# Performance work log

Hardware: AMD Instinct MI355X
Metric: run time of the kernel (lower is better)

The kernel has to match this reference:

```python
import jax, jax.numpy as jnp
import numpy as np

N_NODES = 100_000
N_EDGES = 1_600_000
D_IN, D_HID, N_CLASSES = 128, 128, 40


def setup_inputs() -> dict:
    key = jax.random.key(0)
    ks = jax.random.split(key, 8)
    x = jax.random.normal(ks[0], (N_NODES, D_IN), dtype=jnp.float32)
    edge_index = jax.random.randint(ks[1], (2, N_EDGES), 0, N_NODES, dtype=jnp.int64)
    dims = [(D_IN, D_HID), (D_HID, D_HID), (D_HID, N_CLASSES)]
    inp = {"x": x, "edge_index": edge_index}
    for i, (di, do) in enumerate(dims):
        s = 1.0 / np.sqrt(di)
        inp[f"W_l{i}"] = jax.random.normal(ks[2 + 2 * i], (di, do), dtype=jnp.float32) * s
        inp[f"W_r{i}"] = jax.random.normal(ks[3 + 2 * i], (di, do), dtype=jnp.float32) * s
        inp[f"b{i}"] = jnp.zeros((do,), dtype=jnp.float32)
    return inp


def _sage_conv(x, src, dst, deg_inv, W_l, W_r, b):
    # gather messages from source nodes, mean-aggregate at target nodes
    msg = x[src]                                        # [E, d_in]
    aggr = jax.ops.segment_sum(msg, dst, num_segments=N_NODES) * deg_inv  # [N, d_in]
    return aggr @ W_l + b + x @ W_r                     # [N, d_out]


def reference(x, edge_index, W_l0, W_r0, b0, W_l1, W_r1, b1, W_l2, W_r2, b2):
    src, dst = edge_index[0], edge_index[1]
    deg = jax.ops.segment_sum(jnp.ones((N_EDGES,), x.dtype), dst, num_segments=N_NODES)
    deg_inv = (1.0 / jnp.maximum(deg, 1.0))[:, None]    # [N, 1]

    h = _sage_conv(x, src, dst, deg_inv, W_l0, W_r0, b0)
    h = jax.nn.relu(h)  # dropout p=0.3 is identity in eval mode
    h = _sage_conv(h, src, dst, deg_inv, W_l1, W_r1, b1)
    h = jax.nn.relu(h)
    h = _sage_conv(h, src, dst, deg_inv, W_l2, W_r2, b2)
    return jax.nn.log_softmax(h, axis=1)
```

## Files before the change

### kernel.cpp

```cpp
#include <hip/hip_runtime.h>
#include <math.h>

#define THREADS 256
#define BSHIFT 8
#define BSIZE 256
#define NEB 512

typedef short short8 __attribute__((ext_vector_type(8)));
typedef float f32x4 __attribute__((ext_vector_type(4)));

__device__ __forceinline__ unsigned short f2bf(float f) {
  unsigned u = __builtin_bit_cast(unsigned, f);
  return (unsigned short)((u + 0x7FFFu + ((u >> 16) & 1u)) >> 16);
}
__device__ __forceinline__ float bflo(unsigned u) {
  return __builtin_bit_cast(float, u << 16);
}
__device__ __forceinline__ float bfhi(unsigned u) {
  return __builtin_bit_cast(float, u & 0xFFFF0000u);
}
__device__ __forceinline__ unsigned pack2(float x, float y) {
  return (unsigned)f2bf(x) | ((unsigned)f2bf(y) << 16);
}

__device__ __forceinline__ void acc8(float* a, uint4 u) {
  a[0] += bflo(u.x); a[1] += bfhi(u.x);
  a[2] += bflo(u.y); a[3] += bfhi(u.y);
  a[4] += bflo(u.z); a[5] += bfhi(u.z);
  a[6] += bflo(u.w); a[7] += bfhi(u.w);
}


__global__ __launch_bounds__(256) void k_ehist(const int* __restrict__ dst,
                                               int* __restrict__ cnt_bm,
                                               int E, int chunk, int nbk) {
  __shared__ int h[1024];
  int blk = blockIdx.x, t = threadIdx.x;
  for (int i = t; i < nbk; i += 256) h[i] = 0;
  __syncthreads();
  int e0 = blk * chunk, e1 = min(e0 + chunk, E);
  for (int e = e0 + t; e < e1; e += 256) atomicAdd(&h[dst[e] >> BSHIFT], 1);
  __syncthreads();
  for (int i = t; i < nbk; i += 256) cnt_bm[(size_t)blk * nbk + i] = h[i];
}

__global__ __launch_bounds__(256) void k_bktscan(const int* __restrict__ cnt_bm,
                                                 int* __restrict__ locoff_tm,
                                                 int* __restrict__ bktot, int nbk) {
  int g = blockIdx.x, t = threadIdx.x;
  int c0 = cnt_bm[(size_t)(2 * t) * nbk + g];
  int c1 = cnt_bm[(size_t)(2 * t + 1) * nbk + g];
  __shared__ int sh[256];
  int s = c0 + c1;
  sh[t] = s;
  __syncthreads();
  for (int off = 1; off < 256; off <<= 1) {
    int v = (t >= off) ? sh[t - off] : 0;
    __syncthreads();
    if (t >= off) sh[t] += v;
    __syncthreads();
  }
  int excl = sh[t] - s;
  ((int2*)(locoff_tm + (size_t)g * NEB))[t] = make_int2(excl, excl + c0);
  if (t == 255) bktot[g] = sh[255];
}

__global__ __launch_bounds__(256) void k_topscan(const int* __restrict__ bktot,
                                                 int* __restrict__ bucket_base,
                                                 int nbk, int E,
                                                 int* __restrict__ row_ptr, int N) {
  __shared__ int sums[256];
  int t = threadIdx.x;
  int vals[4];
  int s = 0;
#pragma unroll
  for (int j = 0; j < 4; ++j) {
    int idx = t * 4 + j;
    vals[j] = (idx < nbk) ? bktot[idx] : 0;
    s += vals[j];
  }
  sums[t] = s;
  __syncthreads();
  for (int off = 1; off < 256; off <<= 1) {
    int v = (t >= off) ? sums[t - off] : 0;
    __syncthreads();
    if (t >= off) sums[t] += v;
    __syncthreads();
  }
  int run = sums[t] - s;
#pragma unroll
  for (int j = 0; j < 4; ++j) {
    int idx = t * 4 + j;
    if (idx < nbk) bucket_base[idx] = run;
    run += vals[j];
  }
  if (t == 0) { bucket_base[nbk] = E; row_ptr[N] = E; }
}

__global__ __launch_bounds__(256) void k_eplace(const int* __restrict__ src,
                                                const int* __restrict__ dst,
                                                const int* __restrict__ bucket_base,
                                                const int* __restrict__ locoff_tm,
                                                int* __restrict__ bedge,
                                                int E, int chunk, int nbk) {
  __shared__ int lptr[1024];
  int blk = blockIdx.x, t = threadIdx.x;
  for (int i = t; i < nbk; i += 256)
    lptr[i] = bucket_base[i] + locoff_tm[(size_t)i * NEB + blk];
  __syncthreads();
  int e0 = blk * chunk, e1 = min(e0 + chunk, E);
  for (int e = e0 + t; e < e1; e += 256) {
    int d = dst[e];
    int b = d >> BSHIFT;
    int p = atomicAdd(&lptr[b], 1);
    bedge[p] = (src[e] << 8) | (d & (BSIZE - 1));
  }
}

__global__ __launch_bounds__(256) void k_bcsr2(const int* __restrict__ bedge,
                                               const int* __restrict__ bucket_base,
                                               int* __restrict__ row_ptr,
                                               int* __restrict__ col, int N) {
  int g = blockIdx.x, t = threadIdx.x;
  int beg = bucket_base[g], end = bucket_base[g + 1];
  __shared__ int deg[BSIZE];
  __shared__ int sh[BSIZE];
  __shared__ int cur[BSIZE];
  deg[t] = 0;
  __syncthreads();
  for (int i = beg + t; i < end; i += 256)
    atomicAdd(&deg[bedge[i] & (BSIZE - 1)], 1);
  __syncthreads();
  int s = deg[t];
  sh[t] = s;
  __syncthreads();
  for (int off = 1; off < 256; off <<= 1) {
    int v = (t >= off) ? sh[t - off] : 0;
    __syncthreads();
    if (t >= off) sh[t] += v;
    __syncthreads();
  }
  int ex = beg + sh[t] - s;
  int node = g * BSIZE + t;
  if (node < N) row_ptr[node] = ex;
  cur[t] = ex;
  __syncthreads();
  for (int i = beg + t; i < end; i += 256) {
    int ed = bedge[i];
    int p = atomicAdd(&cur[ed & (BSIZE - 1)], 1);
    col[p] = ed >> 8;
  }
}

__global__ __launch_bounds__(256) void k_wswz_all(
    const float* __restrict__ Wl0, const float* __restrict__ Wr0,
    const float* __restrict__ Wl1, const float* __restrict__ Wr1,
    const float* __restrict__ Wl2, const float* __restrict__ Wr2,
    unsigned short* __restrict__ out0, unsigned short* __restrict__ out1,
    unsigned short* __restrict__ out2) {
  int b = blockIdx.x, t = threadIdx.x;
  if (b < 256) {
    const float* Wl = (b < 128) ? Wl0 : Wl1;
    const float* Wr = (b < 128) ? Wr0 : Wr1;
    unsigned short* out = (b < 128) ? out0 : out1;
    int idx = (b & 127) * 256 + t;
    int j = idx & 7, lane = (idx >> 3) & 63, ct = (idx >> 9) & 15, ks = idx >> 13;
    int k = ks * 32 + (lane >> 4) * 8 + j;
    int c = ct * 16 + (lane & 15);
    float v = (c < 128) ? Wl[k * 128 + c] : Wr[k * 128 + (c - 128)];
    out[idx] = f2bf(v);
  } else {
    int idx = (b - 256) * 256 + t;
    int j = idx & 7, lane = (idx >> 3) & 63;
    int tile = idx >> 9;
    int ct = tile % 5, ks = tile / 5;
    int k = ks * 32 + (lane >> 4) * 8 + j;
    int c = ct * 16 + (lane & 15);
    float v = (c < 40) ? Wl2[k * 40 + c] : ((c < 80) ? Wr2[k * 40 + (c - 40)] : 0.f);
    out2[idx] = f2bf(v);
  }
}

__device__ __forceinline__ void gemm128_body(
    const short8 xf[4], const short8 xg[4],
    const unsigned short* __restrict__ Wswz, const float* __restrict__ bias,
    unsigned short* __restrict__ outL, unsigned short* __restrict__ outR,
    int M, int wave, int lane,
    unsigned short (*lt)[16][136], int rb0) {
  int quad = lane >> 4, n16 = lane & 15;
#pragma unroll
  for (int ct = 0; ct < 8; ++ct) {
    f32x4 accA = {0.f, 0.f, 0.f, 0.f};
    f32x4 accB = {0.f, 0.f, 0.f, 0.f};
    const unsigned short* wp = Wswz + (size_t)(ct * 64 + lane) * 8;
#pragma unroll
    for (int ks = 0; ks < 4; ++ks) {
      short8 wf = *(const short8*)(wp + ks * 8192);
      accA = __builtin_amdgcn_mfma_f32_16x16x32_bf16(wf, xf[ks], accA, 0, 0, 0);
      accB = __builtin_amdgcn_mfma_f32_16x16x32_bf16(wf, xg[ks], accB, 0, 0, 0);
    }
    int ch = ct * 16 + quad * 4;
    ushort4 oA, oB;
    oA.x = f2bf(accA[0]); oA.y = f2bf(accA[1]); oA.z = f2bf(accA[2]); oA.w = f2bf(accA[3]);
    oB.x = f2bf(accB[0]); oB.y = f2bf(accB[1]); oB.z = f2bf(accB[2]); oB.w = f2bf(accB[3]);
    *(ushort4*)&lt[0][n16][ch] = oA;
    *(ushort4*)&lt[1][n16][ch] = oB;
  }
#pragma unroll
  for (int r = 0; r < 4; ++r) {
    int nd = r * 4 + (lane >> 4);
    int ic = (lane & 15) * 8;
    uint4 vA = *(const uint4*)&lt[0][nd][ic];
    uint4 vB = *(const uint4*)&lt[1][nd][ic];
    if (rb0 + nd < M)      *(uint4*)(outL + ((size_t)(rb0 + nd)) * 128 + ic) = vA;
    if (rb0 + 64 + nd < M) *(uint4*)(outL + ((size_t)(rb0 + 64 + nd)) * 128 + ic) = vB;
  }
#pragma unroll
  for (int ct = 8; ct < 16; ++ct) {
    f32x4 accA = {0.f, 0.f, 0.f, 0.f};
    f32x4 accB = {0.f, 0.f, 0.f, 0.f};
    const unsigned short* wp = Wswz + (size_t)(ct * 64 + lane) * 8;
#pragma unroll
    for (int ks = 0; ks < 4; ++ks) {
      short8 wf = *(const short8*)(wp + ks * 8192);
      accA = __builtin_amdgcn_mfma_f32_16x16x32_bf16(wf, xf[ks], accA, 0, 0, 0);
      accB = __builtin_amdgcn_mfma_f32_16x16x32_bf16(wf, xg[ks], accB, 0, 0, 0);
    }
    int ch = (ct - 8) * 16 + quad * 4;
    float4 bv = *(const float4*)(bias + ch);
    ushort4 oA, oB;
    oA.x = f2bf(accA[0] + bv.x); oA.y = f2bf(accA[1] + bv.y);
    oA.z = f2bf(accA[2] + bv.z); oA.w = f2bf(accA[3] + bv.w);
    oB.x = f2bf(accB[0] + bv.x); oB.y = f2bf(accB[1] + bv.y);
    oB.z = f2bf(accB[2] + bv.z); oB.w = f2bf(accB[3] + bv.w);
    *(ushort4*)&lt[0][n16][ch] = oA;
    *(ushort4*)&lt[1][n16][ch] = oB;
  }
#pragma unroll
  for (int r = 0; r < 4; ++r) {
    int nd = r * 4 + (lane >> 4);
    int ic = (lane & 15) * 8;
    uint4 vA = *(const uint4*)&lt[0][nd][ic];
    uint4 vB = *(const uint4*)&lt[1][nd][ic];
    if (rb0 + nd < M)      *(uint4*)(outR + ((size_t)(rb0 + nd)) * 128 + ic) = vA;
    if (rb0 + 64 + nd < M) *(uint4*)(outR + ((size_t)(rb0 + 64 + nd)) * 128 + ic) = vB;
  }
}

__global__ __launch_bounds__(256) void gemm128_mfma_x32(
    const float* __restrict__ X, const unsigned short* __restrict__ Wswz,
    const float* __restrict__ bias,
    unsigned short* __restrict__ outL, unsigned short* __restrict__ outR, int M) {
  __shared__ __align__(16) unsigned short lt[4][2][16][136];
  int wave = threadIdx.x >> 6, lane = threadIdx.x & 63;
  int quad = lane >> 4, n16 = lane & 15;
  int rowA = blockIdx.x * 128 + wave * 16 + n16;
  int rA = min(rowA, M - 1), rB = min(rowA + 64, M - 1);

  short8 xf[4], xg[4];
  const float* xpA = X + (size_t)rA * 128 + quad * 8;
  const float* xpB = X + (size_t)rB * 128 + quad * 8;
#pragma unroll
  for (int ks = 0; ks < 4; ++ks) {
    float4 a0 = *(const float4*)(xpA + ks * 32);
    float4 a1 = *(const float4*)(xpA + ks * 32 + 4);
    float4 b0 = *(const float4*)(xpB + ks * 32);
    float4 b1 = *(const float4*)(xpB + ks * 32 + 4);
    short8 f, g;
    f[0] = (short)f2bf(a0.x); f[1] = (short)f2bf(a0.y);
    f[2] = (short)f2bf(a0.z); f[3] = (short)f2bf(a0.w);
    f[4] = (short)f2bf(a1.x); f[5] = (short)f2bf(a1.y);
    f[6] = (short)f2bf(a1.z); f[7] = (short)f2bf(a1.w);
    g[0] = (short)f2bf(b0.x); g[1] = (short)f2bf(b0.y);
    g[2] = (short)f2bf(b0.z); g[3] = (short)f2bf(b0.w);
    g[4] = (short)f2bf(b1.x); g[5] = (short)f2bf(b1.y);
    g[6] = (short)f2bf(b1.z); g[7] = (short)f2bf(b1.w);
    xf[ks] = f;
    xg[ks] = g;
  }
  gemm128_body(xf, xg, Wswz, bias, outL, outR, M, wave, lane,
               lt[wave], blockIdx.x * 128 + wave * 16);
}

__global__ __launch_bounds__(256) void gemm128_mfma(
    const unsigned short* __restrict__ Xb, const unsigned short* __restrict__ Wswz,
    const float* __restrict__ bias,
    unsigned short* __restrict__ outL, unsigned short* __restrict__ outR, int M) {
  __shared__ __align__(16) unsigned short lt[4][2][16][136];
  int wave = threadIdx.x >> 6, lane = threadIdx.x & 63;
  int quad = lane >> 4, n16 = lane & 15;
  int rowA = blockIdx.x * 128 + wave * 16 + n16;
  int rA = min(rowA, M - 1), rB = min(rowA + 64, M - 1);

  short8 xf[4], xg[4];
  const unsigned short* xpA = Xb + (size_t)rA * 128 + quad * 8;
  const unsigned short* xpB = Xb + (size_t)rB * 128 + quad * 8;
#pragma unroll
  for (int ks = 0; ks < 4; ++ks) {
    xf[ks] = *(const short8*)(xpA + ks * 32);
    xg[ks] = *(const short8*)(xpB + ks * 32);
  }
  gemm128_body(xf, xg, Wswz, bias, outL, outR, M, wave, lane,
               lt[wave], blockIdx.x * 128 + wave * 16);
}

__global__ __launch_bounds__(256) void gemm40_mfma(
    const unsigned short* __restrict__ Xb, const unsigned short* __restrict__ Wswz,
    const float* __restrict__ bias,
    unsigned short* __restrict__ tlb, float* __restrict__ tr, int M) {
  int wave = threadIdx.x >> 6, lane = threadIdx.x & 63;
  int quad = lane >> 4, n16 = lane & 15;
  int row = blockIdx.x * 64 + wave * 16 + n16;
  int row_ld = min(row, M - 1);
  bool ok = row < M;

  short8 xf[4];
  const unsigned short* xp = Xb + (size_t)row_ld * 128 + quad * 8;
#pragma unroll
  for (int ks = 0; ks < 4; ++ks) xf[ks] = *(const short8*)(xp + ks * 32);

#pragma unroll
  for (int ct = 0; ct < 5; ++ct) {
    f32x4 acc = {0.f, 0.f, 0.f, 0.f};
    const unsigned short* wp = Wswz + (size_t)(ct * 64 + lane) * 8;
#pragma unroll
    for (int ks = 0; ks < 4; ++ks) {
      short8 wf = *(const short8*)(wp + (size_t)ks * 5 * 64 * 8);
      acc = __builtin_amdgcn_mfma_f32_16x16x32_bf16(wf, xf[ks], acc, 0, 0, 0);
    }
    int cglob = ct * 16 + quad * 4;
    if (!ok) continue;
    if (cglob < 40) {
      ushort4 o;
      o.x = f2bf(acc[0]); o.y = f2bf(acc[1]); o.z = f2bf(acc[2]); o.w = f2bf(acc[3]);
      *(ushort4*)(tlb + (size_t)row * 64 + cglob) = o;
    } else {
      int c = cglob - 40;
      float4 bv = *(const float4*)(bias + c);
      float4 o;
      o.x = acc[0] + bv.x; o.y = acc[1] + bv.y;
      o.z = acc[2] + bv.z; o.w = acc[3] + bv.w;
      *(float4*)(tr + (size_t)row * 40 + c) = o;
    }
  }
}

__global__ __launch_bounds__(256) void agg128b(
    const unsigned short* __restrict__ xl, const unsigned short* __restrict__ xr,
    const int* __restrict__ row_ptr, const int* __restrict__ col,
    unsigned short* __restrict__ h, int Nn) {
  int wave = threadIdx.x >> 6;
  int lane = threadIdx.x & 63;
  int pair = lane >> 5;
  int l32 = lane & 31;
  int n = blockIdx.x * 4 + wave;
  if (n >= Nn) return;
  int beg = row_ptr[n], end = row_ptr[n + 1];
  int deg = end - beg;
  const uint2* xlq = (const uint2*)xl;
  float a0x = 0.f, a0y = 0.f, a0z = 0.f, a0w = 0.f;
  float a1x = 0.f, a1y = 0.f, a1z = 0.f, a1w = 0.f;
  float a2x = 0.f, a2y = 0.f, a2z = 0.f, a2w = 0.f;
  float a3x = 0.f, a3y = 0.f, a3z = 0.f, a3w = 0.f;
  int e = beg + pair;
  for (int it = deg >> 3; it > 0; --it, e += 8) {
    uint2 u0 = xlq[(size_t)col[e]     * 32 + l32];
    uint2 u1 = xlq[(size_t)col[e + 2] * 32 + l32];
    uint2 u2 = xlq[(size_t)col[e + 4] * 32 + l32];
    uint2 u3 = xlq[(size_t)col[e + 6] * 32 + l32];
    a0x += bflo(u0.x); a0y += bfhi(u0.x); a0z += bflo(u0.y); a0w += bfhi(u0.y);
    a1x += bflo(u1.x); a1y += bfhi(u1.x); a1z += bflo(u1.y); a1w += bfhi(u1.y);
    a2x += bflo(u2.x); a2y += bfhi(u2.x); a2z += bflo(u2.y); a2w += bfhi(u2.y);
    a3x += bflo(u3.x); a3y += bfhi(u3.x); a3z += bflo(u3.y); a3w += bfhi(u3.y);
  }
  for (; e < end; e += 2) {
    uint2 u = xlq[(size_t)col[e] * 32 + l32];
    a0x += bflo(u.x); a0y += bfhi(u.x); a0z += bflo(u.y); a0w += bfhi(u.y);
  }
  float ax = (a0x + a1x) + (a2x + a3x);
  float ay = (a0y + a1y) + (a2y + a3y);
  float az = (a0z + a1z) + (a2z + a3z);
  float aw = (a0w + a1w) + (a2w + a3w);
  ax += __shfl_xor(ax, 32);
  ay += __shfl_xor(ay, 32);
  az += __shfl_xor(az, 32);
  aw += __shfl_xor(aw, 32);
  if (pair == 0) {
    float di = 1.0f / (float)max(deg, 1);
    uint2 r = ((const uint2*)xr)[(size_t)n * 32 + l32];
    float ox = fmaxf(fmaf(ax, di, bflo(r.x)), 0.f);
    float oy = fmaxf(fmaf(ay, di, bfhi(r.x)), 0.f);
    float oz = fmaxf(fmaf(az, di, bflo(r.y)), 0.f);
    float ow = fmaxf(fmaf(aw, di, bfhi(r.y)), 0.f);
    uint2 o;
    o.x = pack2(ox, oy);
    o.y = pack2(oz, ow);
    ((uint2*)h)[(size_t)n * 32 + l32] = o;
  }
}

__global__ __launch_bounds__(256) void agg40_lsm(
    const unsigned short* __restrict__ tlb, const float* __restrict__ tr,
    const int* __restrict__ row_ptr, const int* __restrict__ col,
    float* __restrict__ out, int Nn) {
  int wave = threadIdx.x >> 6;
  int lane = threadIdx.x & 63;
  int ew = lane >> 3;
  int l8 = lane & 7;
  int n = blockIdx.x * 4 + wave;
  if (n >= Nn) return;
  int beg = row_ptr[n], end = row_ptr[n + 1];
  int deg = end - beg;
  const uint4* tlq = (const uint4*)tlb;
  float a0[8], a1[8];
#pragma unroll
  for (int j = 0; j < 8; ++j) { a0[j] = 0.f; a1[j] = 0.f; }
  int rounds = (deg + 15) >> 4;
  if (rounds > 0) {
    int end1 = end - 1;
    int e = beg + ew;
    int c0 = col[min(e, end1)];
    int c1 = col[min(e + 8, end1)];
    for (int it = rounds - 1; it > 0; --it) {
      uint4 u0 = tlq[(size_t)c0 * 8 + l8];
      uint4 u1 = tlq[(size_t)c1 * 8 + l8];
      int en = e + 16;
      int cn0 = col[min(en, end1)];
      int cn1 = col[min(en + 8, end1)];
      acc8(a0, u0); acc8(a1, u1);
      c0 = cn0; c1 = cn1; e = en;
    }
    uint4 u0 = tlq[(size_t)c0 * 8 + l8];
    uint4 u1 = tlq[(size_t)c1 * 8 + l8];
    uint4 z = make_uint4(0u, 0u, 0u, 0u);
    if (e >= end) u0 = z;
    if (e + 8 >= end) u1 = z;
    acc8(a0, u0); acc8(a1, u1);
  }
  float v[8];
#pragma unroll
  for (int j = 0; j < 8; ++j) {
    float t = a0[j] + a1[j];
    t += __shfl_xor(t, 32);
    t += __shfl_xor(t, 16);
    t += __shfl_xor(t, 8);
    v[j] = t;
  }
  bool valid = l8 < 5;
  float di = 1.0f / (float)max(deg, 1);
  float4 r0 = valid ? *(const float4*)(tr + (size_t)n * 40 + 8 * l8)
                    : make_float4(0.f, 0.f, 0.f, 0.f);
  float4 r1 = valid ? *(const float4*)(tr + (size_t)n * 40 + 8 * l8 + 4)
                    : make_float4(0.f, 0.f, 0.f, 0.f);
  float rb[8] = {r0.x, r0.y, r0.z, r0.w, r1.x, r1.y, r1.z, r1.w};
  float vv[8];
#pragma unroll
  for (int j = 0; j < 8; ++j) vv[j] = valid ? fmaf(v[j], di, rb[j]) : -INFINITY;
  float m = vv[0];
#pragma unroll
  for (int j = 1; j < 8; ++j) m = fmaxf(m, vv[j]);
#pragma unroll
  for (int off = 4; off; off >>= 1) m = fmaxf(m, __shfl_xor(m, off));
  float ex = 0.f;
  if (valid) {
#pragma unroll
    for (int j = 0; j < 8; ++j) ex += expf(vv[j] - m);
  }
  float ssum = ex;
#pragma unroll
  for (int off = 4; off; off >>= 1) ssum += __shfl_xor(ssum, off);
  float lg = logf(ssum);
  if (ew == 0 && valid) {
    float4 o0, o1;
    o0.x = (vv[0] - m) - lg; o0.y = (vv[1] - m) - lg;
    o0.z = (vv[2] - m) - lg; o0.w = (vv[3] - m) - lg;
    o1.x = (vv[4] - m) - lg; o1.y = (vv[5] - m) - lg;
    o1.z = (vv[6] - m) - lg; o1.w = (vv[7] - m) - lg;
    *(float4*)(out + (size_t)n * 40 + 8 * l8) = o0;
    *(float4*)(out + (size_t)n * 40 + 8 * l8 + 4) = o1;
  }
}


extern "C" void kernel_launch(void* const* d_in, const int* in_sizes, int n_in,
                              void* d_out, int out_size, void* d_ws, size_t ws_size,
                              hipStream_t stream) {
  const float* x   = (const float*)d_in[0];
  const int*   ei  = (const int*)d_in[1];
  const float* Wl0 = (const float*)d_in[2];
  const float* Wr0 = (const float*)d_in[3];
  const float* b0  = (const float*)d_in[4];
  const float* Wl1 = (const float*)d_in[5];
  const float* Wr1 = (const float*)d_in[6];
  const float* b1  = (const float*)d_in[7];
  const float* Wl2 = (const float*)d_in[8];
  const float* Wr2 = (const float*)d_in[9];
  const float* b2  = (const float*)d_in[10];

  int N = in_sizes[0] / 128;
  int E = in_sizes[1] / 2;
  const int* src = ei;
  const int* dst = ei + E;
  int nbk = (N + BSIZE - 1) / BSIZE;
  int chunk = (E + NEB - 1) / NEB;

  char* ws = (char*)d_ws;
  size_t off = 0;
  auto alloc = [&](size_t bytes) -> void* {
    void* p = ws + off;
    off += (bytes + 255) & ~(size_t)255;
    return p;
  };
  unsigned short* gA  = (unsigned short*)alloc((size_t)N * 128 * 2);
  unsigned short* gB  = (unsigned short*)alloc((size_t)N * 128 * 2);
  unsigned short* hC  = (unsigned short*)alloc((size_t)N * 128 * 2);
  unsigned short* tlb = (unsigned short*)alloc((size_t)N * 64 * 2);
  float* tr           = (float*)alloc((size_t)N * 40 * 4);
  int* row_ptr  = (int*)alloc((size_t)(N + 1) * 4);
  int* col      = (int*)alloc((size_t)E * 4);
  int* bedge    = (int*)alloc((size_t)E * 4);
  int* cnt_bm   = (int*)alloc((size_t)NEB * nbk * 4);
  int* locoff   = (int*)alloc((size_t)nbk * NEB * 4);
  int* bktot    = (int*)alloc((size_t)nbk * 4);
  int* bbase    = (int*)alloc((size_t)(nbk + 1) * 4);
  unsigned short* wswz0 = (unsigned short*)alloc(32768 * 2);
  unsigned short* wswz1 = (unsigned short*)alloc(32768 * 2);
  unsigned short* wswz2 = (unsigned short*)alloc(10240 * 2);
  (void)ws_size; (void)n_in; (void)out_size;

  k_ehist<<<NEB, 256, 0, stream>>>(dst, cnt_bm, E, chunk, nbk);
  k_bktscan<<<nbk, 256, 0, stream>>>(cnt_bm, locoff, bktot, nbk);
  k_topscan<<<1, 256, 0, stream>>>(bktot, bbase, nbk, E, row_ptr, N);
  k_eplace<<<NEB, 256, 0, stream>>>(src, dst, bbase, locoff, bedge, E, chunk, nbk);
  k_bcsr2<<<nbk, 256, 0, stream>>>(bedge, bbase, row_ptr, col, N);

  k_wswz_all<<<296, 256, 0, stream>>>(Wl0, Wr0, Wl1, Wr1, Wl2, Wr2,
                                      wswz0, wswz1, wswz2);

  int gg128 = (N + 127) / 128;
  int gg = (N + 63) / 64;
  int nb = (N + 3) / 4;

  gemm128_mfma_x32<<<gg128, 256, 0, stream>>>(x, wswz0, b0, gA, gB, N);
  agg128b<<<nb, 256, 0, stream>>>(gA, gB, row_ptr, col, hC, N);
  gemm128_mfma<<<gg128, 256, 0, stream>>>(hC, wswz1, b1, gA, gB, N);
  agg128b<<<nb, 256, 0, stream>>>(gA, gB, row_ptr, col, hC, N);
  gemm40_mfma<<<gg, 256, 0, stream>>>(hC, wswz2, b2, tlb, tr, N);
  agg40_lsm<<<nb, 256, 0, stream>>>(tlb, tr, row_ptr, col, (float*)d_out, N);
}
```

Baseline: 417.4 us.

## Merge CSR build stages with weight swizzle and first GEMM, shrink final table

Independent preprocessing stages now share launches. The destination histogram and weight swizzle run in one kernel, and the per-bucket scan and first-layer GEMM run in another. The top-level scan is folded into the edge-placement kernel, where every block recomputes it redundantly. The final-layer bf16 neighbor table is also narrowed from 64 to 40 columns per row, cutting gather bytes. This reduces launch count and idle gaps between small kernels, at the cost of heterogeneous blocks per launch and unaligned 80-byte row strides in the last gather.

Measured after the change: 400.2 us. -4.1%, faster.

```diff
diff --git a/kernel.cpp b/kernel.cpp
--- a/kernel.cpp
+++ b/kernel.cpp
@@ -30,89 +30,207 @@
   a[6] += bflo(u.w); a[7] += bfhi(u.w);
 }
 
-
-__global__ __launch_bounds__(256) void k_ehist(const int* __restrict__ dst,
-                                               int* __restrict__ cnt_bm,
-                                               int E, int chunk, int nbk) {
-  __shared__ int h[1024];
+__device__ __forceinline__ void gemm128_body(
+    const short8 xf[4], const short8 xg[4],
+    const unsigned short* __restrict__ Wswz, const float* __restrict__ bias,
+    unsigned short* __restrict__ outL, unsigned short* __restrict__ outR,
+    int M, int lane,
+    unsigned short (*lt)[16][136], int rb0) {
+  int quad = lane >> 4, n16 = lane & 15;
+#pragma unroll
+  for (int ct = 0; ct < 8; ++ct) {
+    f32x4 accA = {0.f, 0.f, 0.f, 0.f};
+    f32x4 accB = {0.f, 0.f, 0.f, 0.f};
+    const unsigned short* wp = Wswz + (size_t)(ct * 64 + lane) * 8;
+#pragma unroll
+    for (int ks = 0; ks < 4; ++ks) {
+      short8 wf = *(const short8*)(wp + ks * 8192);
+      accA = __builtin_amdgcn_mfma_f32_16x16x32_bf16(wf, xf[ks], accA, 0, 0, 0);
+      accB = __builtin_amdgcn_mfma_f32_16x16x32_bf16(wf, xg[ks], accB, 0, 0, 0);
+    }
+    int ch = ct * 16 + quad * 4;
+    ushort4 oA, oB;
+    oA.x = f2bf(accA[0]); oA.y = f2bf(accA[1]); oA.z = f2bf(accA[2]); oA.w = f2bf(accA[3]);
+    oB.x = f2bf(accB[0]); oB.y = f2bf(accB[1]); oB.z = f2bf(accB[2]); oB.w = f2bf(accB[3]);
+    *(ushort4*)&lt[0][n16][ch] = oA;
+    *(ushort4*)&lt[1][n16][ch] = oB;
+  }
+#pragma unroll
+  for (int r = 0; r < 4; ++r) {
+    int nd = r * 4 + (lane >> 4);
+    int ic = (lane & 15) * 8;
+    uint4 vA = *(const uint4*)&lt[0][nd][ic];
+    uint4 vB = *(const uint4*)&lt[1][nd][ic];
+    if (rb0 + nd < M)      *(uint4*)(outL + ((size_t)(rb0 + nd)) * 128 + ic) = vA;
+    if (rb0 + 64 + nd < M) *(uint4*)(outL + ((size_t)(rb0 + 64 + nd)) * 128 + ic) = vB;
+  }
+#pragma unroll
+  for (int ct = 8; ct < 16; ++ct) {
+    f32x4 accA = {0.f, 0.f, 0.f, 0.f};
+    f32x4 accB = {0.f, 0.f, 0.f, 0.f};
+    const unsigned short* wp = Wswz + (size_t)(ct * 64 + lane) * 8;
+#pragma unroll
+    for (int ks = 0; ks < 4; ++ks) {
+      short8 wf = *(const short8*)(wp + ks * 8192);
+      accA = __builtin_amdgcn_mfma_f32_16x16x32_bf16(wf, xf[ks], accA, 0, 0, 0);
+      accB = __builtin_amdgcn_mfma_f32_16x16x32_bf16(wf, xg[ks], accB, 0, 0, 0);
+    }
+    int ch = (ct - 8) * 16 + quad * 4;
+    float4 bv = *(const float4*)(bias + ch);
+    ushort4 oA, oB;
+    oA.x = f2bf(accA[0] + bv.x); oA.y = f2bf(accA[1] + bv.y);
+    oA.z = f2bf(accA[2] + bv.z); oA.w = f2bf(accA[3] + bv.w);
+    oB.x = f2bf(accB[0] + bv.x); oB.y = f2bf(accB[1] + bv.y);
+    oB.z = f2bf(accB[2] + bv.z); oB.w = f2bf(accB[3] + bv.w);
+    *(ushort4*)&lt[0][n16][ch] = oA;
+    *(ushort4*)&lt[1][n16][ch] = oB;
+  }
+#pragma unroll
+  for (int r = 0; r < 4; ++r) {
+    int nd = r * 4 + (lane >> 4);
+    int ic = (lane & 15) * 8;
+    uint4 vA = *(const uint4*)&lt[0][nd][ic];
+    uint4 vB = *(const uint4*)&lt[1][nd][ic];
+    if (rb0 + nd < M)      *(uint4*)(outR + ((size_t)(rb0 + nd)) * 128 + ic) = vA;
+    if (rb0 + 64 + nd < M) *(uint4*)(outR + ((size_t)(rb0 + 64 + nd)) * 128 + ic) = vB;
+  }
+}
+
+__global__ __launch_bounds__(256) void k_phase0(
+    const int* __restrict__ dst, int* __restrict__ cnt_bm, int E, int chunk, int nbk,
+    const float* __restrict__ Wl0, const float* __restrict__ Wr0,
+    const float* __restrict__ Wl1, const float* __restrict__ Wr1,
+    const float* __restrict__ Wl2, const float* __restrict__ Wr2,
+    unsigned short* __restrict__ out0, unsigned short* __restrict__ out1,
+    unsigned short* __restrict__ out2) {
+  int b = blockIdx.x, t = threadIdx.x;
+  if (b < NEB) {
+    __shared__ int h[1024];
+    for (int i = t; i < nbk; i += 256) h[i] = 0;
+    __syncthreads();
+    int e0 = b * chunk, e1 = min(e0 + chunk, E);
+    for (int e = e0 + t; e < e1; e += 256) atomicAdd(&h[dst[e] >> BSHIFT], 1);
+    __syncthreads();
+    for (int i = t; i < nbk; i += 256) cnt_bm[(size_t)b * nbk + i] = h[i];
+    return;
+  }
+  int wb = b - NEB;
+  if (wb < 256) {
+    const float* Wl = (wb < 128) ? Wl0 : Wl1;
+    const float* Wr = (wb < 128) ? Wr0 : Wr1;
+    unsigned short* out = (wb < 128) ? out0 : out1;
+    int idx = (wb & 127) * 256 + t;
+    int j = idx & 7, lane = (idx >> 3) & 63, ct = (idx >> 9) & 15, ks = idx >> 13;
+    int k = ks * 32 + (lane >> 4) * 8 + j;
+    int c = ct * 16 + (lane & 15);
+    float v = (c < 128) ? Wl[k * 128 + c] : Wr[k * 128 + (c - 128)];
+    out[idx] = f2bf(v);
+  } else {
+    int idx = (wb - 256) * 256 + t;
+    int j = idx & 7, lane = (idx >> 3) & 63;
+    int tile = idx >> 9;
+    int ct = tile % 5, ks = tile / 5;
+    int k = ks * 32 + (lane >> 4) * 8 + j;
+    int c = ct * 16 + (lane & 15);
+    float v = (c < 40) ? Wl2[k * 40 + c] : ((c < 80) ? Wr2[k * 40 + (c - 40)] : 0.f);
+    out2[idx] = f2bf(v);
+  }
+}
+
+__global__ __launch_bounds__(256) void k_phase1(
+    const int* __restrict__ cnt_bm, int* __restrict__ locoff_tm,
+    int* __restrict__ bktot, int nbk,
+    const float* __restrict__ X, const unsigned short* __restrict__ Wswz,
+    const float* __restrict__ bias,
+    unsigned short* __restrict__ outL, unsigned short* __restrict__ outR, int M) {
+  __shared__ int sh[256];
+  __shared__ __align__(16) unsigned short lt[4][2][16][136];
+  int t = threadIdx.x;
+  if (blockIdx.x < (unsigned)nbk) {
+    int g = blockIdx.x;
+    int c0 = cnt_bm[(size_t)(2 * t) * nbk + g];
+    int c1 = cnt_bm[(size_t)(2 * t + 1) * nbk + g];
+    int s = c0 + c1;
+    sh[t] = s;
+    __syncthreads();
+    for (int off = 1; off < 256; off <<= 1) {
+      int v = (t >= off) ? sh[t - off] : 0;
+      __syncthreads();
+      if (t >= off) sh[t] += v;
+      __syncthreads();
+    }
+    int excl = sh[t] - s;
+    ((int2*)(locoff_tm + (size_t)g * NEB))[t] = make_int2(excl, excl + c0);
+    if (t == 255) bktot[g] = sh[255];
+    return;
+  }
+  int gb = blockIdx.x - nbk;
+  int wave = t >> 6, lane = t & 63;
+  int quad = lane >> 4, n16 = lane & 15;
+  int rowA = gb * 128 + wave * 16 + n16;
+  int rA = min(rowA, M - 1), rB = min(rowA + 64, M - 1);
+
+  short8 xf[4], xg[4];
+  const float* xpA = X + (size_t)rA * 128 + quad * 8;
+  const float* xpB = X + (size_t)rB * 128 + quad * 8;
+#pragma unroll
+  for (int ks = 0; ks < 4; ++ks) {
+    float4 a0 = *(const float4*)(xpA + ks * 32);
+    float4 a1 = *(const float4*)(xpA + ks * 32 + 4);
+    float4 b0 = *(const float4*)(xpB + ks * 32);
+    float4 b1 = *(const float4*)(xpB + ks * 32 + 4);
+    short8 f, g;
+    f[0] = (short)f2bf(a0.x); f[1] = (short)f2bf(a0.y);
+    f[2] = (short)f2bf(a0.z); f[3] = (short)f2bf(a0.w);
+    f[4] = (short)f2bf(a1.x); f[5] = (short)f2bf(a1.y);
+    f[6] = (short)f2bf(a1.z); f[7] = (short)f2bf(a1.w);
+    g[0] = (short)f2bf(b0.x); g[1] = (short)f2bf(b0.y);
+    g[2] = (short)f2bf(b0.z); g[3] = (short)f2bf(b0.w);
+    g[4] = (short)f2bf(b1.x); g[5] = (short)f2bf(b1.y);
+    g[6] = (short)f2bf(b1.z); g[7] = (short)f2bf(b1.w);
+    xf[ks] = f;
+    xg[ks] = g;
+  }
+  gemm128_body(xf, xg, Wswz, bias, outL, outR, M, lane,
+               lt[wave], gb * 128 + wave * 16);
+}
+
+__global__ __launch_bounds__(256) void k_eplace2(
+    const int* __restrict__ src, const int* __restrict__ dst,
+    const int* __restrict__ bktot, const int* __restrict__ locoff_tm,
+    int* __restrict__ bedge, int* __restrict__ bucket_base,
+    int* __restrict__ row_ptr,
+    int E, int chunk, int nbk, int N) {
+  __shared__ int lptr[1024];
+  __shared__ int psum[256];
   int blk = blockIdx.x, t = threadIdx.x;
-  for (int i = t; i < nbk; i += 256) h[i] = 0;
-  __syncthreads();
-  int e0 = blk * chunk, e1 = min(e0 + chunk, E);
-  for (int e = e0 + t; e < e1; e += 256) atomicAdd(&h[dst[e] >> BSHIFT], 1);
-  __syncthreads();
-  for (int i = t; i < nbk; i += 256) cnt_bm[(size_t)blk * nbk + i] = h[i];
-}
-
-__global__ __launch_bounds__(256) void k_bktscan(const int* __restrict__ cnt_bm,
-                                                 int* __restrict__ locoff_tm,
-                                                 int* __restrict__ bktot, int nbk) {
-  int g = blockIdx.x, t = threadIdx.x;
-  int c0 = cnt_bm[(size_t)(2 * t) * nbk + g];
-  int c1 = cnt_bm[(size_t)(2 * t + 1) * nbk + g];
-  __shared__ int sh[256];
-  int s = c0 + c1;
-  sh[t] = s;
+  int v0 = (2 * t < nbk) ? bktot[2 * t] : 0;
+  int v1 = (2 * t + 1 < nbk) ? bktot[2 * t + 1] : 0;
+  int s = v0 + v1;
+  psum[t] = s;
   __syncthreads();
   for (int off = 1; off < 256; off <<= 1) {
-    int v = (t >= off) ? sh[t - off] : 0;
-    __syncthreads();
-    if (t >= off) sh[t] += v;
-    __syncthreads();
-  }
-  int excl = sh[t] - s;
-  ((int2*)(locoff_tm + (size_t)g * NEB))[t] = make_int2(excl, excl + c0);
-  if (t == 255) bktot[g] = sh[255];
-}
-
-__global__ __launch_bounds__(256) void k_topscan(const int* __restrict__ bktot,
-                                                 int* __restrict__ bucket_base,
-                                                 int nbk, int E,
-                                                 int* __restrict__ row_ptr, int N) {
-  __shared__ int sums[256];
-  int t = threadIdx.x;
-  int vals[4];
-  int s = 0;
-#pragma unroll
-  for (int j = 0; j < 4; ++j) {
-    int idx = t * 4 + j;
-    vals[j] = (idx < nbk) ? bktot[idx] : 0;
-    s += vals[j];
-  }
-  sums[t] = s;
-  __syncthreads();
-  for (int off = 1; off < 256; off <<= 1) {
-    int v = (t >= off) ? sums[t - off] : 0;
-    __syncthreads();
-    if (t >= off) sums[t] += v;
-    __syncthreads();
-  }
-  int run = sums[t] - s;
-#pragma unroll
-  for (int j = 0; j < 4; ++j) {
-    int idx = t * 4 + j;
-    if (idx < nbk) bucket_base[idx] = run;
-    run += vals[j];
-  }
-  if (t == 0) { bucket_base[nbk] = E; row_ptr[N] = E; }
-}
-
-__global__ __launch_bounds__(256) void k_eplace(const int* __restrict__ src,
-                                                const int* __restrict__ dst,
-                                                const int* __restrict__ bucket_base,
-                                                const int* __restrict__ locoff_tm,
-                                                int* __restrict__ bedge,
-                                                int E, int chunk, int nbk) {
-  __shared__ int lptr[1024];
-  int blk = blockIdx.x, t = threadIdx.x;
-  for (int i = t; i < nbk; i += 256)
-    lptr[i] = bucket_base[i] + locoff_tm[(size_t)i * NEB + blk];
+    int v = (t >= off) ? psum[t - off] : 0;
+    __syncthreads();
+    if (t >= off) psum[t] += v;
+    __syncthreads();
+  }
+  int excl = psum[t] - s;
+  if (2 * t < nbk)
+    lptr[2 * t] = excl + locoff_tm[(size_t)(2 * t) * NEB + blk];
+  if (2 * t + 1 < nbk)
+    lptr[2 * t + 1] = excl + v0 + locoff_tm[(size_t)(2 * t + 1) * NEB + blk];
+  if (blk == 0) {
+    if (2 * t < nbk)     bucket_base[2 * t] = excl;
+    if (2 * t + 1 < nbk) bucket_base[2 * t + 1] = excl + v0;
+    if (t == 0) { bucket_base[nbk] = E; row_ptr[N] = E; }
+  }
   __syncthreads();
   int e0 = blk * chunk, e1 = min(e0 + chunk, E);
   for (int e = e0 + t; e < e1; e += 256) {
     int d = dst[e];
-    int b = d >> BSHIFT;
-    int p = atomicAdd(&lptr[b], 1);
+    int bkt = d >> BSHIFT;
+    int p = atomicAdd(&lptr[bkt], 1);
     bedge[p] = (src[e] << 8) | (d & (BSIZE - 1));
   }
 }
@@ -152,136 +270,6 @@
   }
 }
 
-__global__ __launch_bounds__(256) void k_wswz_all(
-    const float* __restrict__ Wl0, const float* __restrict__ Wr0,
-    const float* __restrict__ Wl1, const float* __restrict__ Wr1,
-    const float* __restrict__ Wl2, const float* __restrict__ Wr2,
-    unsigned short* __restrict__ out0, unsigned short* __restrict__ out1,
-    unsigned short* __restrict__ out2) {
-  int b = blockIdx.x, t = threadIdx.x;
-  if (b < 256) {
-    const float* Wl = (b < 128) ? Wl0 : Wl1;
-    const float* Wr = (b < 128) ? Wr0 : Wr1;
-    unsigned short* out = (b < 128) ? out0 : out1;
-    int idx = (b & 127) * 256 + t;
-    int j = idx & 7, lane = (idx >> 3) & 63, ct = (idx >> 9) & 15, ks = idx >> 13;
-    int k = ks * 32 + (lane >> 4) * 8 + j;
-    int c = ct * 16 + (lane & 15);
-    float v = (c < 128) ? Wl[k * 128 + c] : Wr[k * 128 + (c - 128)];
-    out[idx] = f2bf(v);
-  } else {
-    int idx = (b - 256) * 256 + t;
-    int j = idx & 7, lane = (idx >> 3) & 63;
-    int tile = idx >> 9;
-    int ct = tile % 5, ks = tile / 5;
-    int k = ks * 32 + (lane >> 4) * 8 + j;
-    int c = ct * 16 + (lane & 15);
-    float v = (c < 40) ? Wl2[k * 40 + c] : ((c < 80) ? Wr2[k * 40 + (c - 40)] : 0.f);
-    out2[idx] = f2bf(v);
-  }
-}
-
-__device__ __forceinline__ void gemm128_body(
-    const short8 xf[4], const short8 xg[4],
-    const unsigned short* __restrict__ Wswz, const float* __restrict__ bias,
-    unsigned short* __restrict__ outL, unsigned short* __restrict__ outR,
-    int M, int wave, int lane,
-    unsigned short (*lt)[16][136], int rb0) {
-  int quad = lane >> 4, n16 = lane & 15;
-#pragma unroll
-  for (int ct = 0; ct < 8; ++ct) {
-    f32x4 accA = {0.f, 0.f, 0.f, 0.f};
-    f32x4 accB = {0.f, 0.f, 0.f, 0.f};
-    const unsigned short* wp = Wswz + (size_t)(ct * 64 + lane) * 8;
-#pragma unroll
-    for (int ks = 0; ks < 4; ++ks) {
-      short8 wf = *(const short8*)(wp + ks * 8192);
-      accA = __builtin_amdgcn_mfma_f32_16x16x32_bf16(wf, xf[ks], accA, 0, 0, 0);
-      accB = __builtin_amdgcn_mfma_f32_16x16x32_bf16(wf, xg[ks], accB, 0, 0, 0);
-    }
-    int ch = ct * 16 + quad * 4;
-    ushort4 oA, oB;
-    oA.x = f2bf(accA[0]); oA.y = f2bf(accA[1]); oA.z = f2bf(accA[2]); oA.w = f2bf(accA[3]);
-    oB.x = f2bf(accB[0]); oB.y = f2bf(accB[1]); oB.z = f2bf(accB[2]); oB.w = f2bf(accB[3]);
-    *(ushort4*)&lt[0][n16][ch] = oA;
-    *(ushort4*)&lt[1][n16][ch] = oB;
-  }
-#pragma unroll
-  for (int r = 0; r < 4; ++r) {
-    int nd = r * 4 + (lane >> 4);
-    int ic = (lane & 15) * 8;
-    uint4 vA = *(const uint4*)&lt[0][nd][ic];
-    uint4 vB = *(const uint4*)&lt[1][nd][ic];
-    if (rb0 + nd < M)      *(uint4*)(outL + ((size_t)(rb0 + nd)) * 128 + ic) = vA;
-    if (rb0 + 64 + nd < M) *(uint4*)(outL + ((size_t)(rb0 + 64 + nd)) * 128 + ic) = vB;
-  }
-#pragma unroll
-  for (int ct = 8; ct < 16; ++ct) {
-    f32x4 accA = {0.f, 0.f, 0.f, 0.f};
-    f32x4 accB = {0.f, 0.f, 0.f, 0.f};
-    const unsigned short* wp = Wswz + (size_t)(ct * 64 + lane) * 8;
-#pragma unroll
-    for (int ks = 0; ks < 4; ++ks) {
-      short8 wf = *(const short8*)(wp + ks * 8192);
-      accA = __builtin_amdgcn_mfma_f32_16x16x32_bf16(wf, xf[ks], accA, 0, 0, 0);
-      accB = __builtin_amdgcn_mfma_f32_16x16x32_bf16(wf, xg[ks], accB, 0, 0, 0);
-    }
-    int ch = (ct - 8) * 16 + quad * 4;
-    float4 bv = *(const float4*)(bias + ch);
-    ushort4 oA, oB;
-    oA.x = f2bf(accA[0] + bv.x); oA.y = f2bf(accA[1] + bv.y);
-    oA.z = f2bf(accA[2] + bv.z); oA.w = f2bf(accA[3] + bv.w);
-    oB.x = f2bf(accB[0] + bv.x); oB.y = f2bf(accB[1] + bv.y);
-    oB.z = f2bf(accB[2] + bv.z); oB.w = f2bf(accB[3] + bv.w);
-    *(ushort4*)&lt[0][n16][ch] = oA;
-    *(ushort4*)&lt[1][n16][ch] = oB;
-  }
-#pragma unroll
-  for (int r = 0; r < 4; ++r) {
-    int nd = r * 4 + (lane >> 4);
-    int ic = (lane & 15) * 8;
-    uint4 vA = *(const uint4*)&lt[0][nd][ic];
-    uint4 vB = *(const uint4*)&lt[1][nd][ic];
-    if (rb0 + nd < M)      *(uint4*)(outR + ((size_t)(rb0 + nd)) * 128 + ic) = vA;
-    if (rb0 + 64 + nd < M) *(uint4*)(outR + ((size_t)(rb0 + 64 + nd)) * 128 + ic) = vB;
-  }
-}
-
-__global__ __launch_bounds__(256) void gemm128_mfma_x32(
-    const float* __restrict__ X, const unsigned short* __restrict__ Wswz,
-    const float* __restrict__ bias,
-    unsigned short* __restrict__ outL, unsigned short* __restrict__ outR, int M) {
-  __shared__ __align__(16) unsigned short lt[4][2][16][136];
-  int wave = threadIdx.x >> 6, lane = threadIdx.x & 63;
-  int quad = lane >> 4, n16 = lane & 15;
-  int rowA = blockIdx.x * 128 + wave * 16 + n16;
-  int rA = min(rowA, M - 1), rB = min(rowA + 64, M - 1);
-
-  short8 xf[4], xg[4];
-  const float* xpA = X + (size_t)rA * 128 + quad * 8;
-  const float* xpB = X + (size_t)rB * 128 + quad * 8;
-#pragma unroll
-  for (int ks = 0; ks < 4; ++ks) {
-    float4 a0 = *(const float4*)(xpA + ks * 32);
-    float4 a1 = *(const float4*)(xpA + ks * 32 + 4);
-    float4 b0 = *(const float4*)(xpB + ks * 32);
-    float4 b1 = *(const float4*)(xpB + ks * 32 + 4);
-    short8 f, g;
-    f[0] = (short)f2bf(a0.x); f[1] = (short)f2bf(a0.y);
-    f[2] = (short)f2bf(a0.z); f[3] = (short)f2bf(a0.w);
-    f[4] = (short)f2bf(a1.x); f[5] = (short)f2bf(a1.y);
-    f[6] = (short)f2bf(a1.z); f[7] = (short)f2bf(a1.w);
-    g[0] = (short)f2bf(b0.x); g[1] = (short)f2bf(b0.y);
-    g[2] = (short)f2bf(b0.z); g[3] = (short)f2bf(b0.w);
-    g[4] = (short)f2bf(b1.x); g[5] = (short)f2bf(b1.y);
-    g[6] = (short)f2bf(b1.z); g[7] = (short)f2bf(b1.w);
-    xf[ks] = f;
-    xg[ks] = g;
-  }
-  gemm128_body(xf, xg, Wswz, bias, outL, outR, M, wave, lane,
-               lt[wave], blockIdx.x * 128 + wave * 16);
-}
-
 __global__ __launch_bounds__(256) void gemm128_mfma(
     const unsigned short* __restrict__ Xb, const unsigned short* __restrict__ Wswz,
     const float* __restrict__ bias,
@@ -300,7 +288,7 @@
     xf[ks] = *(const short8*)(xpA + ks * 32);
     xg[ks] = *(const short8*)(xpB + ks * 32);
   }
-  gemm128_body(xf, xg, Wswz, bias, outL, outR, M, wave, lane,
+  gemm128_body(xf, xg, Wswz, bias, outL, outR, M, lane,
                lt[wave], blockIdx.x * 128 + wave * 16);
 }
 
@@ -333,7 +321,7 @@
     if (cglob < 40) {
       ushort4 o;
       o.x = f2bf(acc[0]); o.y = f2bf(acc[1]); o.z = f2bf(acc[2]); o.w = f2bf(acc[3]);
-      *(ushort4*)(tlb + (size_t)row * 64 + cglob) = o;
+      *(ushort4*)(tlb + (size_t)row * 40 + cglob) = o;
     } else {
       int c = cglob - 40;
       float4 bv = *(const float4*)(bias + c);
@@ -422,16 +410,16 @@
     int c0 = col[min(e, end1)];
     int c1 = col[min(e + 8, end1)];
     for (int it = rounds - 1; it > 0; --it) {
-      uint4 u0 = tlq[(size_t)c0 * 8 + l8];
-      uint4 u1 = tlq[(size_t)c1 * 8 + l8];
+      uint4 u0 = tlq[(size_t)c0 * 5 + l8];
+      uint4 u1 = tlq[(size_t)c1 * 5 + l8];
       int en = e + 16;
       int cn0 = col[min(en, end1)];
       int cn1 = col[min(en + 8, end1)];
       acc8(a0, u0); acc8(a1, u1);
       c0 = cn0; c1 = cn1; e = en;
     }
-    uint4 u0 = tlq[(size_t)c0 * 8 + l8];
-    uint4 u1 = tlq[(size_t)c1 * 8 + l8];
+    uint4 u0 = tlq[(size_t)c0 * 5 + l8];
+    uint4 u1 = tlq[(size_t)c1 * 5 + l8];
     uint4 z = make_uint4(0u, 0u, 0u, 0u);
     if (e >= end) u0 = z;
     if (e + 8 >= end) u1 = z;
@@ -514,7 +502,7 @@
   unsigned short* gA  = (unsigned short*)alloc((size_t)N * 128 * 2);
   unsigned short* gB  = (unsigned short*)alloc((size_t)N * 128 * 2);
   unsigned short* hC  = (unsigned short*)alloc((size_t)N * 128 * 2);
-  unsigned short* tlb = (unsigned short*)alloc((size_t)N * 64 * 2);
+  unsigned short* tlb = (unsigned short*)alloc((size_t)N * 40 * 2);
   float* tr           = (float*)alloc((size_t)N * 40 * 4);
   int* row_ptr  = (int*)alloc((size_t)(N + 1) * 4);
   int* col      = (int*)alloc((size_t)E * 4);
@@ -528,20 +516,19 @@
   unsigned short* wswz2 = (unsigned short*)alloc(10240 * 2);
   (void)ws_size; (void)n_in; (void)out_size;
 
-  k_ehist<<<NEB, 256, 0, stream>>>(dst, cnt_bm, E, chunk, nbk);
-  k_bktscan<<<nbk, 256, 0, stream>>>(cnt_bm, locoff, bktot, nbk);
-  k_topscan<<<1, 256, 0, stream>>>(bktot, bbase, nbk, E, row_ptr, N);
-  k_eplace<<<NEB, 256, 0, stream>>>(src, dst, bbase, locoff, bedge, E, chunk, nbk);
-  k_bcsr2<<<nbk, 256, 0, stream>>>(bedge, bbase, row_ptr, col, N);
-
-  k_wswz_all<<<296, 256, 0, stream>>>(Wl0, Wr0, Wl1, Wr1, Wl2, Wr2,
-                                      wswz0, wswz1, wswz2);
-
   int gg128 = (N + 127) / 128;
   int gg = (N + 63) / 64;
   int nb = (N + 3) / 4;
 
-  gemm128_mfma_x32<<<gg128, 256, 0, stream>>>(x, wswz0, b0, gA, gB, N);
+  k_phase0<<<NEB + 296, 256, 0, stream>>>(dst, cnt_bm, E, chunk, nbk,
+                                          Wl0, Wr0, Wl1, Wr1, Wl2, Wr2,
+                                          wswz0, wswz1, wswz2);
+  k_phase1<<<nbk + gg128, 256, 0, stream>>>(cnt_bm, locoff, bktot, nbk,
+                                            x, wswz0, b0, gA, gB, N);
+  k_eplace2<<<NEB, 256, 0, stream>>>(src, dst, bktot, locoff, bedge, bbase,
+                                     row_ptr, E, chunk, nbk, N);
+  k_bcsr2<<<nbk, 256, 0, stream>>>(bedge, bbase, row_ptr, col, N);
+
   agg128b<<<nb, 256, 0, stream>>>(gA, gB, row_ptr, col, hC, N);
   gemm128_mfma<<<gg128, 256, 0, stream>>>(hC, wswz1, b1, gA, gB, N);
   agg128b<<<nb, 256, 0, stream>>>(gA, gB, row_ptr, col, hC, N);
```
